# Kernel tuning notes

Hardware: AMD Instinct MI355X
Metric: run time of the kernel (lower is better)

## Reference

```python
import jax, jax.numpy as jnp
import numpy as np
import math

EMBED_DIM = 1024
NUM_HEADS = 16
HEAD_DIM = EMBED_DIM // NUM_HEADS
BATCH = 2
SEQ = 2048


def setup_inputs() -> dict:
    key = jax.random.key(0)
    ks = jax.random.split(key, 9)
    s = 1.0 / math.sqrt(EMBED_DIM)
    return {
        "x": jax.random.normal(ks[0], (BATCH, SEQ, EMBED_DIM), jnp.float32),
        "Wq": jax.random.normal(ks[1], (EMBED_DIM, EMBED_DIM), jnp.float32) * s,
        "bq": jnp.zeros((EMBED_DIM,), jnp.float32),
        "Wk": jax.random.normal(ks[2], (EMBED_DIM, EMBED_DIM), jnp.float32) * s,
        "bk": jnp.zeros((EMBED_DIM,), jnp.float32),
        "Wv": jax.random.normal(ks[3], (EMBED_DIM, EMBED_DIM), jnp.float32) * s,
        "bv": jnp.zeros((EMBED_DIM,), jnp.float32),
        "Wo": jax.random.normal(ks[4], (EMBED_DIM, EMBED_DIM), jnp.float32) * s,
        "bo": jnp.zeros((EMBED_DIM,), jnp.float32),
    }


def _rope_tables(seq_len, dim, dtype):
    inv_freq = 1.0 / (10000.0 ** (jnp.arange(0, dim, 2, dtype=jnp.float32) / dim))
    t = jnp.arange(seq_len, dtype=jnp.float32)
    freqs = jnp.einsum("i,j->ij", t, inv_freq)          # [S, D/2]
    emb = jnp.concatenate([freqs, freqs], axis=-1)       # [S, D]
    return jnp.cos(emb).astype(dtype), jnp.sin(emb).astype(dtype)


def _rotate_half(x):
    x1, x2 = jnp.split(x, 2, axis=-1)
    return jnp.concatenate([-x2, x1], axis=-1)


def _apply_rope(x, cos, sin):
    # x: [B, S, H, D]; cos/sin: [S, D] -> broadcast over batch & heads
    cos = cos[None, :, None, :]
    sin = sin[None, :, None, :]
    return x * cos + _rotate_half(x) * sin


def reference(x, Wq, bq, Wk, bk, Wv, bv, Wo, bo):
    B, S, E = x.shape
    H, D = NUM_HEADS, HEAD_DIM
    q = (x @ Wq + bq).reshape(B, S, H, D)
    k = (x @ Wk + bk).reshape(B, S, H, D)
    v = (x @ Wv + bv).reshape(B, S, H, D)
    cos, sin = _rope_tables(S, D, x.dtype)
    q = _apply_rope(q, cos, sin)
    k = _apply_rope(k, cos, sin)
    scale = 1.0 / math.sqrt(D)
    # scores: [B, H, S, S]
    scores = jnp.einsum("bqhd,bkhd->bhqk", q, k) * scale
    attn = jax.nn.softmax(scores, axis=-1)
    ctx = jnp.einsum("bhqk,bkhd->bqhd", attn, v).reshape(B, S, E)
    return ctx @ Wo + bo
```

## Files before the change

kernel.cpp:

```cpp
#include <hip/hip_runtime.h>
#include <math.h>

#define B_ 2
#define S_ 2048
#define E_ 1024
#define H_ 16
#define D_ 64
#define M_ (B_*S_)

typedef _Float16 f16x8  __attribute__((ext_vector_type(8)));
typedef _Float16 f16x4v __attribute__((ext_vector_type(4)));
typedef __fp16   h16x2  __attribute__((ext_vector_type(2)));
typedef float    f32x4  __attribute__((ext_vector_type(4)));

__device__ __forceinline__ ushort f2h(float f) {
    _Float16 h = (_Float16)f;
    return __builtin_bit_cast(ushort, h);
}

__device__ __forceinline__ void gload_lds16(const ushort* g, ushort* l) {
    __builtin_amdgcn_global_load_lds(
        (const __attribute__((address_space(1))) unsigned int*)g,
        (__attribute__((address_space(3))) unsigned int*)l, 16, 0, 0);
}

__device__ __forceinline__ float exp2_fast(float x) {
    return __builtin_amdgcn_exp2f(x);
}

__global__ void prep_kernel(const float* __restrict__ x,
                            const float* __restrict__ W0, const float* __restrict__ W1,
                            const float* __restrict__ W2, const float* __restrict__ W3,
                            ushort* __restrict__ xf, ushort* __restrict__ WT,
                            float* __restrict__ ct, float* __restrict__ st)
{
    const int bid = blockIdx.x;
    const int tid = threadIdx.x;
    __shared__ float tile[32][33];

    if (bid < 2048) {
        const int z = bid >> 9, rem = bid & 511;
        const int kp = rem >> 5, nb = (rem & 31) * 32;
        const float* W = (z == 0) ? W0 : (z == 1) ? W1 : (z == 2) ? W2 : W3;
        const size_t zoff = (size_t)z * E_ * E_;
        const int tx = tid & 31, ty = tid >> 5;
        #pragma unroll
        for (int kk = 0; kk < 2; kk++) {
            const int k0 = kp * 64 + kk * 32;
            #pragma unroll
            for (int i = 0; i < 4; i++) {
                int r = i * 8 + ty;
                tile[r][tx] = W[(size_t)(k0 + r) * E_ + nb + tx];
            }
            __syncthreads();
            #pragma unroll
            for (int i = 0; i < 4; i++) {
                int r = i * 8 + ty;
                WT[zoff + (size_t)(nb + r) * E_ + k0 + tx] = f2h(tile[tx][r]);
            }
            __syncthreads();
        }
    } else if (bid < 3072) {
        const int base = (bid - 2048) * 4096 + tid * 4;
        #pragma unroll
        for (int j = 0; j < 4; j++) {
            const int i = base + j * 1024;
            float4 v = *(const float4*)&x[i];
            *(ushort4*)&xf[i] = make_ushort4(f2h(v.x), f2h(v.y), f2h(v.z), f2h(v.w));
        }
    } else {
        const int i = (bid - 3072) * 256 + tid;
        const int j = i & 31, pos = i >> 5;
        float invf = (float)pow(10000.0, -(double)j / 32.0);
        float ang  = (float)pos * invf;
        ct[i] = (float)cos((double)ang);
        st[i] = (float)sin((double)ang);
    }
}

#define GBM 128
#define GBN 128
#define GBK 32
#define LOG2E 1.44269504088896340736f

__global__ __launch_bounds__(256, 3)
void gemm_f16(const ushort* __restrict__ A, const ushort* __restrict__ WTp,
              const float* __restrict__ b0, const float* __restrict__ b1,
              const float* __restrict__ b2,
              const float* __restrict__ ct, const float* __restrict__ st,
              ushort* __restrict__ outQ, ushort* __restrict__ outK,
              ushort* __restrict__ outV)
{
    __shared__ __align__(16) ushort lA[3][GBM * GBK];
    __shared__ __align__(16) ushort lB[3][GBN * GBK];

    const int tid  = threadIdx.x;
    const int wv   = tid >> 6, lane = tid & 63;
    const int c    = lane & 15, qd = lane >> 4;
    const int rh   = wv >> 1, chn = wv & 1;

    const int mode = (int)blockIdx.z;
    const size_t zoff = (size_t)blockIdx.z * (E_ * E_);
    const ushort* Bt = WTp + zoff;

    const int m0 = (blockIdx.x & 31) * GBM;
    const int n0 = (blockIdx.x >> 5) * GBN;

    const ushort* gsrc = (wv < 2) ? A : Bt;
    const int rowbase = ((wv < 2) ? m0 : n0) + (wv & 1) * 64;
    const int lofs = (wv & 1) * 64 * GBK;
    const int srow = lane >> 2;
    const int soct = (lane & 3) * 8;

    f32x4 acc[4][4] = {};

    #pragma unroll
    for (int pt = 0; pt < 2; pt++) {
        ushort* dst = ((wv < 2) ? &lA[pt][0] : &lB[pt][0]) + lofs;
        const int k0i = pt * GBK;
        #pragma unroll
        for (int cc = 0; cc < 4; cc++) {
            const ushort* g = gsrc + (size_t)(rowbase + cc * 16 + srow) * E_ + k0i + soct;
            gload_lds16(g, dst + cc * 512);
        }
    }
    __builtin_amdgcn_s_waitcnt(0x0F74);
    __builtin_amdgcn_s_barrier();

    for (int t = 0; t < E_ / GBK; t++) {
        if (t + 2 < E_ / GBK) {
            const int bi = (t + 2) % 3;
            const int k0i = (t + 2) * GBK;
            ushort* dst = ((wv < 2) ? &lA[bi][0] : &lB[bi][0]) + lofs;
            #pragma unroll
            for (int cc = 0; cc < 4; cc++) {
                const ushort* g = gsrc + (size_t)(rowbase + cc * 16 + srow) * E_ + k0i + soct;
                gload_lds16(g, dst + cc * 512);
            }
        }

        const ushort* Ab = lA[t % 3];
        const ushort* Bb = lB[t % 3];

        f16x8 af[4], bf[4];
        #pragma unroll
        for (int mt = 0; mt < 4; mt++)
            af[mt] = *(const f16x8*)&Ab[(rh * 64 + mt * 16 + c) * GBK + qd * 8];
        #pragma unroll
        for (int nt = 0; nt < 4; nt++)
            bf[nt] = *(const f16x8*)&Bb[(chn * 64 + nt * 16 + c) * GBK + qd * 8];
        #pragma unroll
        for (int mt = 0; mt < 4; mt++)
            #pragma unroll
            for (int nt = 0; nt < 4; nt++)
                acc[mt][nt] = __builtin_amdgcn_mfma_f32_16x16x32_f16(af[mt], bf[nt], acc[mt][nt], 0, 0, 0);

        if (t < E_ / GBK - 2) {
            __builtin_amdgcn_s_waitcnt(0x0F74);
            __builtin_amdgcn_s_barrier();
        } else if (t == E_ / GBK - 2) {
            __builtin_amdgcn_s_waitcnt(0x0F70);
            __builtin_amdgcn_s_barrier();
        }
    }

    const float* bias = (mode == 0) ? b0 : (mode == 1) ? b1 : b2;
    const int colbase = n0 + chn * 64;

    if (mode == 2) {
        const int hd = colbase >> 6;
        const int xr = (c >> 2) & 3;
        #pragma unroll
        for (int mt = 0; mt < 4; mt++)
            #pragma unroll
            for (int r = 0; r < 4; r++) {
                const int row = m0 + rh * 64 + mt * 16 + qd * 4 + r;
                const int bb = row >> 11, sl = row & (S_ - 1);
                const int g  = sl >> 5, k32 = sl & 31;
                const int q2 = (k32 >> 2) & 3, kh = k32 >> 4, kj = k32 & 3;
                const size_t base = (size_t)(bb * H_ + hd) * (S_ * D_)
                                  + g * 2048 + ((q2 ^ xr) << 3) + kh * 4 + kj;
                #pragma unroll
                for (int nt = 0; nt < 4; nt++) {
                    const int d = nt * 16 + c;
                    outV[base + (size_t)d * 32] = f2h(acc[mt][nt][r] + bias[colbase + d]);
                }
            }
    } else {
        ushort* O = (mode == 0) ? outQ : outK;
        const float sc = (mode == 0) ? 0.125f * LOG2E : 1.0f;
        #pragma unroll
        for (int mt = 0; mt < 4; mt++)
            #pragma unroll
            for (int r = 0; r < 4; r++) {
                const int row = m0 + rh * 64 + mt * 16 + qd * 4 + r;
                const int pos = row & (S_ - 1);
                const int sw = row & 7;
                #pragma unroll
                for (int p = 0; p < 2; p++) {
                    const int j32 = p * 16 + c;
                    const float cth = ct[pos * 32 + j32], sth = st[pos * 32 + j32];
                    const float v1 = acc[mt][p][r]     + bias[colbase + p * 16 + c];
                    const float v2 = acc[mt][p + 2][r] + bias[colbase + (p + 2) * 16 + c];
                    const float o1 = (v1 * cth - v2 * sth) * sc;
                    const float o2 = (v2 * cth + v1 * sth) * sc;
                    const int cd1 = p * 16 + c, cd2 = cd1 + 32;
                    O[(size_t)row * E_ + colbase + (((cd1 >> 3) ^ sw) * 8) + (cd1 & 7)] = f2h(o1);
                    O[(size_t)row * E_ + colbase + (((cd2 >> 3) ^ sw) * 8) + (cd2 & 7)] = f2h(o2);
                }
            }
    }
}

__global__ __launch_bounds__(256, 3)
void gemm_proj(const ushort* __restrict__ A, const ushort* __restrict__ WTp,
               const float* __restrict__ bo, float* __restrict__ outF)
{
    __shared__ __align__(16) ushort lA[3][64 * GBK];
    __shared__ __align__(16) ushort lB[3][GBN * GBK];

    const int tid  = threadIdx.x;
    const int wv   = tid >> 6, lane = tid & 63;
    const int c    = lane & 15, qd = lane >> 4;

    const int m0 = (blockIdx.x & 63) * 64;
    const int n0 = (blockIdx.x >> 6) * GBN;

    const bool stager = (wv < 3);
    const ushort* gsrc = (wv == 0) ? A : WTp;
    const int rowbase = (wv == 0) ? m0 : (n0 + (wv - 1) * 64);
    const int lofs = (wv == 0) ? 0 : (wv - 1) * 64 * GBK;
    const int srow = lane >> 2;
    const int soct = (lane & 3) * 8;

    f32x4 acc[4][2] = {};

    #pragma unroll
    for (int pt = 0; pt < 2; pt++) {
        if (stager) {
            ushort* dst = ((wv == 0) ? &lA[pt][0] : &lB[pt][0]) + lofs;
            const int k0i = pt * GBK;
            #pragma unroll
            for (int cc = 0; cc < 4; cc++) {
                const ushort* g = gsrc + (size_t)(rowbase + cc * 16 + srow) * E_ + k0i + soct;
                gload_lds16(g, dst + cc * 512);
            }
        }
    }
    __builtin_amdgcn_s_waitcnt(0x0F74);
    __builtin_amdgcn_s_barrier();

    for (int t = 0; t < E_ / GBK; t++) {
        if (t + 2 < E_ / GBK && stager) {
            const int bi = (t + 2) % 3;
            const int k0i = (t + 2) * GBK;
            ushort* dst = ((wv == 0) ? &lA[bi][0] : &lB[bi][0]) + lofs;
            #pragma unroll
            for (int cc = 0; cc < 4; cc++) {
                const ushort* g = gsrc + (size_t)(rowbase + cc * 16 + srow) * E_ + k0i + soct;
                gload_lds16(g, dst + cc * 512);
            }
        }

        const ushort* Ab = lA[t % 3];
        const ushort* Bb = lB[t % 3];

        f16x8 af[4], bf[2];
        #pragma unroll
        for (int mt = 0; mt < 4; mt++)
            af[mt] = *(const f16x8*)&Ab[(mt * 16 + c) * GBK + qd * 8];
        #pragma unroll
        for (int nt = 0; nt < 2; nt++)
            bf[nt] = *(const f16x8*)&Bb[(wv * 32 + nt * 16 + c) * GBK + qd * 8];
        #pragma unroll
        for (int mt = 0; mt < 4; mt++)
            #pragma unroll
            for (int nt = 0; nt < 2; nt++)
                acc[mt][nt] = __builtin_amdgcn_mfma_f32_16x16x32_f16(af[mt], bf[nt], acc[mt][nt], 0, 0, 0);

        if (t < E_ / GBK - 2) {
            __builtin_amdgcn_s_waitcnt(0x0F74);
            __builtin_amdgcn_s_barrier();
        } else if (t == E_ / GBK - 2) {
            __builtin_amdgcn_s_waitcnt(0x0F70);
            __builtin_amdgcn_s_barrier();
        }
    }

    #pragma unroll
    for (int mt = 0; mt < 4; mt++)
        #pragma unroll
        for (int r = 0; r < 4; r++) {
            const int row = m0 + mt * 16 + qd * 4 + r;
            #pragma unroll
            for (int nt = 0; nt < 2; nt++) {
                const int col = n0 + wv * 32 + nt * 16 + c;
                outF[(size_t)row * E_ + col] = acc[mt][nt][r] + bo[col];
            }
        }
}

__global__ __launch_bounds__(256, 3)
void attn_mfma(const ushort* __restrict__ Qf, const ushort* __restrict__ Kf,
               const ushort* __restrict__ Vfg, ushort* __restrict__ ctxf)
{
    __shared__ __align__(16) ushort L[24576];

    const int tid = threadIdx.x;
    const int wv = tid >> 6, lane = tid & 63;
    const int c = lane & 15, qd = lane >> 4;
    const int cs = c & 7;

    const int xcd = blockIdx.x & 7, ii = blockIdx.x >> 3;
    const int bh = xcd * 4 + (ii & 3);
    const int qtb = ii >> 2;
    const int b = bh >> 4, h = bh & 15;
    const int q0 = qtb * 64;

    const size_t qrow0 = (size_t)b * S_ + q0;
    const size_t krow0 = (size_t)b * S_;
    const size_t vbase = (size_t)bh * (S_ * D_);

    const int l8 = lane >> 3, l7 = lane & 7;

    #pragma unroll
    for (int j = 0; j < 2; j++) {
        const int row = wv * 16 + j * 8 + l8;
        gload_lds16(Qf + (qrow0 + row) * E_ + h * 64 + l7 * 8, &L[wv * 1024 + j * 512]);
    }
    __syncthreads();
    f16x8 qfrag[4][2];
    #pragma unroll
    for (int qt = 0; qt < 4; qt++)
        #pragma unroll
        for (int kc = 0; kc < 2; kc++)
            qfrag[qt][kc] = *(const f16x8*)&L[(qt * 16 + c) * 64 + (((kc * 4 + qd) ^ cs) * 8)];
    __syncthreads();

    f32x4 acc[4][4] = {};
    float lsum[4] = {0.f, 0.f, 0.f, 0.f};

    ushort* const myL = &L[wv * 6144];
    const int vxo = (qd ^ ((c >> 2) & 3)) << 3;

    const ushort* kst0 = Kf + (krow0 + wv * 32 + l8) * E_ + h * 64 + l7 * 8;
    const ushort* kst1 = kst0 + 8 * E_;
    const ushort* vstA = Vfg + vbase + (size_t)wv * 2048 + lane * 8;
    const ushort* vstB = vstA + 512;

    gload_lds16(kst0, myL);
    gload_lds16(kst1, myL + 512);
    gload_lds16(vstA, myL + 2048);
    gload_lds16(vstB, myL + 2560);
    kst0 += 16 * E_; kst1 += 16 * E_; vstA += 1024; vstB += 1024;

    #pragma unroll 1
    for (int T = 0; T < 16; T++) {
        uint4 bfu[4];

        {
            ushort* vd = myL + 2048 + (T & 1) * 2048 + 1024;
            gload_lds16(kst0, myL + 1024);
            gload_lds16(kst1, myL + 1536);
            gload_lds16(vstA, vd);
            gload_lds16(vstB, vd + 512);
            kst0 += 112 * E_; kst1 += 112 * E_; vstA += 7168; vstB += 7168;
            __builtin_amdgcn_s_waitcnt(0x0F74);

            const ushort* kb = myL;
            f16x8 kf0 = *(const f16x8*)&kb[c * 64 + ((qd ^ cs) * 8)];
            f16x8 kf1 = *(const f16x8*)&kb[c * 64 + (((4 + qd) ^ cs) * 8)];
            f32x4 sv[4];
            __builtin_amdgcn_s_setprio(1);
            #pragma unroll
            for (int qt = 0; qt < 4; qt++) {
                f32x4 s = {};
                s = __builtin_amdgcn_mfma_f32_16x16x32_f16(kf0, qfrag[qt][0], s, 0, 0, 0);
                sv[qt] = __builtin_amdgcn_mfma_f32_16x16x32_f16(kf1, qfrag[qt][1], s, 0, 0, 0);
            }
            __builtin_amdgcn_s_setprio(0);
            #pragma unroll
            for (int qt = 0; qt < 4; qt++) {
                const float p0 = exp2_fast(sv[qt][0]), p1 = exp2_fast(sv[qt][1]);
                const float p2 = exp2_fast(sv[qt][2]), p3 = exp2_fast(sv[qt][3]);
                lsum[qt] += (p0 + p1) + (p2 + p3);
                bfu[qt].x = __builtin_bit_cast(unsigned int, __builtin_amdgcn_cvt_pkrtz(p0, p1));
                bfu[qt].y = __builtin_bit_cast(unsigned int, __builtin_amdgcn_cvt_pkrtz(p2, p3));
            }
        }

        {
            if (T < 15) {
                ushort* vd = myL + 2048 + ((T + 1) & 1) * 2048;
                gload_lds16(kst0, myL);
                gload_lds16(kst1, myL + 512);
                gload_lds16(vstA, vd);
                gload_lds16(vstB, vd + 512);
                kst0 += 16 * E_; kst1 += 16 * E_; vstA += 1024; vstB += 1024;
                __builtin_amdgcn_s_waitcnt(0x0F74);
            } else {
                __builtin_amdgcn_s_waitcnt(0x0F70);
            }

            const ushort* kb = myL + 1024;
            f16x8 kf0 = *(const f16x8*)&kb[c * 64 + ((qd ^ cs) * 8)];
            f16x8 kf1 = *(const f16x8*)&kb[c * 64 + (((4 + qd) ^ cs) * 8)];
            f32x4 sv[4];
            __builtin_amdgcn_s_setprio(1);
            #pragma unroll
            for (int qt = 0; qt < 4; qt++) {
                f32x4 s = {};
                s = __builtin_amdgcn_mfma_f32_16x16x32_f16(kf0, qfrag[qt][0], s, 0, 0, 0);
                sv[qt] = __builtin_amdgcn_mfma_f32_16x16x32_f16(kf1, qfrag[qt][1], s, 0, 0, 0);
            }
            __builtin_amdgcn_s_setprio(0);
            #pragma unroll
            for (int qt = 0; qt < 4; qt++) {
                const float p0 = exp2_fast(sv[qt][0]), p1 = exp2_fast(sv[qt][1]);
                const float p2 = exp2_fast(sv[qt][2]), p3 = exp2_fast(sv[qt][3]);
                lsum[qt] += (p0 + p1) + (p2 + p3);
                bfu[qt].z = __builtin_bit_cast(unsigned int, __builtin_amdgcn_cvt_pkrtz(p0, p1));
                bfu[qt].w = __builtin_bit_cast(unsigned int, __builtin_amdgcn_cvt_pkrtz(p2, p3));
            }
        }

        const ushort* vb = myL + 2048 + (T & 1) * 2048;
        __builtin_amdgcn_s_setprio(1);
        #pragma unroll
        for (int dt = 0; dt < 4; dt++) {
            f16x8 vfr = *(const f16x8*)&vb[(dt * 16 + c) * 32 + vxo];
            #pragma unroll
            for (int qt = 0; qt < 4; qt++)
                acc[dt][qt] = __builtin_amdgcn_mfma_f32_16x16x32_f16(
                    vfr, __builtin_bit_cast(f16x8, bfu[qt]), acc[dt][qt], 0, 0, 0);
        }
        __builtin_amdgcn_s_setprio(0);
    }

    __syncthreads();

    float* red = (float*)&L[0];
    float* lsr = (float*)&L[8192];

    #pragma unroll
    for (int qt = 0; qt < 4; qt++) {
        float v = lsum[qt];
        v += __shfl_xor(v, 16);
        v += __shfl_xor(v, 32);
        lsum[qt] = v;
    }
    if (lane < 16) {
        #pragma unroll
        for (int qt = 0; qt < 4; qt++) lsr[wv * 64 + qt * 16 + lane] = lsum[qt];
    }

    f32x4 own[4];
    #pragma unroll
    for (int qt = 0; qt < 4; qt++)
        own[qt] = (wv == 0) ? acc[0][qt] : (wv == 1) ? acc[1][qt]
                : (wv == 2) ? acc[2][qt] : acc[3][qt];

    #pragma unroll
    for (int r = 1; r < 4; r++) {
        const int ds = (wv + r) & 3;
        #pragma unroll
        for (int qt = 0; qt < 4; qt++) {
            f32x4 sv = (ds == 0) ? acc[0][qt] : (ds == 1) ? acc[1][qt]
                     : (ds == 2) ? acc[2][qt] : acc[3][qt];
            *(f32x4*)&red[ds * 1024 + qt * 256 + lane * 4] = sv;
        }
        __syncthreads();
        #pragma unroll
        for (int qt = 0; qt < 4; qt++)
            own[qt] += *(const f32x4*)&red[wv * 1024 + qt * 256 + lane * 4];
        if (r < 3) __syncthreads();
    }

    float inv[4];
    #pragma unroll
    for (int qt = 0; qt < 4; qt++) {
        const int q = qt * 16 + c;
        inv[qt] = 1.0f / (lsr[q] + lsr[64 + q] + lsr[128 + q] + lsr[192 + q]);
    }

    const size_t obase = qrow0 * E_ + h * 64 + wv * 16 + qd * 4;
    #pragma unroll
    for (int qt = 0; qt < 4; qt++) {
        f32x4 v = own[qt];
        const float iq = inv[qt];
        ushort4 o = make_ushort4(f2h(v[0] * iq), f2h(v[1] * iq),
                                 f2h(v[2] * iq), f2h(v[3] * iq));
        *(ushort4*)&ctxf[obase + (size_t)(qt * 16 + c) * E_] = o;
    }
}

extern "C" void kernel_launch(void* const* d_in, const int* in_sizes, int n_in,
                              void* d_out, int out_size, void* d_ws, size_t ws_size,
                              hipStream_t stream)
{
    const float* x  = (const float*)d_in[0];
    const float* Wq = (const float*)d_in[1];
    const float* bq = (const float*)d_in[2];
    const float* Wk = (const float*)d_in[3];
    const float* bk = (const float*)d_in[4];
    const float* Wv = (const float*)d_in[5];
    const float* bv = (const float*)d_in[6];
    const float* Wo = (const float*)d_in[7];
    const float* bo = (const float*)d_in[8];
    float* out = (float*)d_out;

    ushort* Qb = (ushort*)d_ws;
    ushort* Kb = Qb + (size_t)M_ * E_;
    ushort* Vf = Kb + (size_t)M_ * E_;
    ushort* xf = Vf + (size_t)M_ * E_;
    ushort* WT = xf + (size_t)M_ * E_;
    float*  ct = (float*)(WT + (size_t)4 * E_ * E_);
    float*  st = ct + S_ * 32;
    ushort* ctxf = Qb;

    hipLaunchKernelGGL(prep_kernel, dim3(3328), dim3(256), 0, stream,
                       x, Wq, Wk, Wv, Wo, xf, WT, ct, st);

    hipLaunchKernelGGL(gemm_f16, dim3(256, 1, 3), dim3(256), 0, stream,
                       xf, WT, bq, bk, bv, ct, st,
                       Qb, Kb, Vf);

    hipLaunchKernelGGL(attn_mfma, dim3(B_ * H_ * (S_ / 64)), dim3(256), 0, stream,
                       Qb, Kb, Vf, ctxf);

    hipLaunchKernelGGL(gemm_proj, dim3(512), dim3(256), 0, stream,
                       ctxf, WT + (size_t)3 * E_ * E_, bo, out);
}
```

Measured before the change: 180.8 us.

## Halve attention query tile to 32 rows and single-buffer V for higher occupancy

The attention kernel now processes 32 query rows per block instead of 64, which doubles the grid. The V tile moves from double to single buffering, cutting LDS per block from 48KB to 32KB and raising launch bounds to 4 blocks per CU. The next V tile is now loaded only after the PV MFMAs finish, which exposes V load latency within each iteration. Each K/V tile is also reused across fewer queries, so K and V global/L2 traffic doubles. The intent is better latency hiding through occupancy, traded against less reuse.

```diff
diff --git a/kernel.cpp b/kernel.cpp
--- a/kernel.cpp
+++ b/kernel.cpp
@@ -300,11 +300,11 @@
         }
 }
 
-__global__ __launch_bounds__(256, 3)
+__global__ __launch_bounds__(256, 4)
 void attn_mfma(const ushort* __restrict__ Qf, const ushort* __restrict__ Kf,
                const ushort* __restrict__ Vfg, ushort* __restrict__ ctxf)
 {
-    __shared__ __align__(16) ushort L[24576];
+    __shared__ __align__(16) ushort L[16384];
 
     const int tid = threadIdx.x;
     const int wv = tid >> 6, lane = tid & 63;
@@ -315,7 +315,7 @@
     const int bh = xcd * 4 + (ii & 3);
     const int qtb = ii >> 2;
     const int b = bh >> 4, h = bh & 15;
-    const int q0 = qtb * 64;
+    const int q0 = qtb * 32;
 
     const size_t qrow0 = (size_t)b * S_ + q0;
     const size_t krow0 = (size_t)b * S_;
@@ -323,24 +323,20 @@
 
     const int l8 = lane >> 3, l7 = lane & 7;
 
-    #pragma unroll
-    for (int j = 0; j < 2; j++) {
-        const int row = wv * 16 + j * 8 + l8;
-        gload_lds16(Qf + (qrow0 + row) * E_ + h * 64 + l7 * 8, &L[wv * 1024 + j * 512]);
-    }
+    gload_lds16(Qf + (qrow0 + wv * 8 + l8) * E_ + h * 64 + l7 * 8, &L[wv * 512]);
     __syncthreads();
-    f16x8 qfrag[4][2];
-    #pragma unroll
-    for (int qt = 0; qt < 4; qt++)
+    f16x8 qfrag[2][2];
+    #pragma unroll
+    for (int qt = 0; qt < 2; qt++)
         #pragma unroll
         for (int kc = 0; kc < 2; kc++)
             qfrag[qt][kc] = *(const f16x8*)&L[(qt * 16 + c) * 64 + (((kc * 4 + qd) ^ cs) * 8)];
     __syncthreads();
 
-    f32x4 acc[4][4] = {};
-    float lsum[4] = {0.f, 0.f, 0.f, 0.f};
-
-    ushort* const myL = &L[wv * 6144];
+    f32x4 acc[4][2] = {};
+    float lsum[2] = {0.f, 0.f};
+
+    ushort* const myL = &L[wv * 4096];
     const int vxo = (qd ^ ((c >> 2) & 3)) << 3;
 
     const ushort* kst0 = Kf + (krow0 + wv * 32 + l8) * E_ + h * 64 + l7 * 8;
@@ -350,37 +346,38 @@
 
     gload_lds16(kst0, myL);
     gload_lds16(kst1, myL + 512);
+    kst0 += 16 * E_; kst1 += 16 * E_;
     gload_lds16(vstA, myL + 2048);
     gload_lds16(vstB, myL + 2560);
-    kst0 += 16 * E_; kst1 += 16 * E_; vstA += 1024; vstB += 1024;
+    vstA += 1024; vstB += 1024;
+    gload_lds16(vstA, myL + 3072);
+    gload_lds16(vstB, myL + 3584);
+    vstA += 7168; vstB += 7168;
 
     #pragma unroll 1
     for (int T = 0; T < 16; T++) {
-        uint4 bfu[4];
+        uint4 bfu[2];
 
         {
-            ushort* vd = myL + 2048 + (T & 1) * 2048 + 1024;
             gload_lds16(kst0, myL + 1024);
             gload_lds16(kst1, myL + 1536);
-            gload_lds16(vstA, vd);
-            gload_lds16(vstB, vd + 512);
-            kst0 += 112 * E_; kst1 += 112 * E_; vstA += 7168; vstB += 7168;
-            __builtin_amdgcn_s_waitcnt(0x0F74);
+            kst0 += 112 * E_; kst1 += 112 * E_;
+            __builtin_amdgcn_s_waitcnt(0x0F76);
 
             const ushort* kb = myL;
             f16x8 kf0 = *(const f16x8*)&kb[c * 64 + ((qd ^ cs) * 8)];
             f16x8 kf1 = *(const f16x8*)&kb[c * 64 + (((4 + qd) ^ cs) * 8)];
-            f32x4 sv[4];
+            f32x4 sv[2];
             __builtin_amdgcn_s_setprio(1);
             #pragma unroll
-            for (int qt = 0; qt < 4; qt++) {
+            for (int qt = 0; qt < 2; qt++) {
                 f32x4 s = {};
                 s = __builtin_amdgcn_mfma_f32_16x16x32_f16(kf0, qfrag[qt][0], s, 0, 0, 0);
                 sv[qt] = __builtin_amdgcn_mfma_f32_16x16x32_f16(kf1, qfrag[qt][1], s, 0, 0, 0);
             }
             __builtin_amdgcn_s_setprio(0);
             #pragma unroll
-            for (int qt = 0; qt < 4; qt++) {
+            for (int qt = 0; qt < 2; qt++) {
                 const float p0 = exp2_fast(sv[qt][0]), p1 = exp2_fast(sv[qt][1]);
                 const float p2 = exp2_fast(sv[qt][2]), p3 = exp2_fast(sv[qt][3]);
                 lsum[qt] += (p0 + p1) + (p2 + p3);
@@ -391,13 +388,10 @@
 
         {
             if (T < 15) {
-                ushort* vd = myL + 2048 + ((T + 1) & 1) * 2048;
                 gload_lds16(kst0, myL);
                 gload_lds16(kst1, myL + 512);
-                gload_lds16(vstA, vd);
-                gload_lds16(vstB, vd + 512);
-                kst0 += 16 * E_; kst1 += 16 * E_; vstA += 1024; vstB += 1024;
-                __builtin_amdgcn_s_waitcnt(0x0F74);
+                kst0 += 16 * E_; kst1 += 16 * E_;
+                __builtin_amdgcn_s_waitcnt(0x0F72);
             } else {
                 __builtin_amdgcn_s_waitcnt(0x0F70);
             }
@@ -405,17 +399,17 @@
             const ushort* kb = myL + 1024;
             f16x8 kf0 = *(const f16x8*)&kb[c * 64 + ((qd ^ cs) * 8)];
             f16x8 kf1 = *(const f16x8*)&kb[c * 64 + (((4 + qd) ^ cs) * 8)];
-            f32x4 sv[4];
+            f32x4 sv[2];
             __builtin_amdgcn_s_setprio(1);
             #pragma unroll
-            for (int qt = 0; qt < 4; qt++) {
+            for (int qt = 0; qt < 2; qt++) {
                 f32x4 s = {};
                 s = __builtin_amdgcn_mfma_f32_16x16x32_f16(kf0, qfrag[qt][0], s, 0, 0, 0);
                 sv[qt] = __builtin_amdgcn_mfma_f32_16x16x32_f16(kf1, qfrag[qt][1], s, 0, 0, 0);
             }
             __builtin_amdgcn_s_setprio(0);
             #pragma unroll
-            for (int qt = 0; qt < 4; qt++) {
+            for (int qt = 0; qt < 2; qt++) {
                 const float p0 = exp2_fast(sv[qt][0]), p1 = exp2_fast(sv[qt][1]);
                 const float p2 = exp2_fast(sv[qt][2]), p3 = exp2_fast(sv[qt][3]);
                 lsum[qt] += (p0 + p1) + (p2 + p3);
@@ -424,26 +418,36 @@
             }
         }
 
-        const ushort* vb = myL + 2048 + (T & 1) * 2048;
+        const ushort* vb = myL + 2048;
         __builtin_amdgcn_s_setprio(1);
         #pragma unroll
         for (int dt = 0; dt < 4; dt++) {
             f16x8 vfr = *(const f16x8*)&vb[(dt * 16 + c) * 32 + vxo];
-            #pragma unroll
-            for (int qt = 0; qt < 4; qt++)
-                acc[dt][qt] = __builtin_amdgcn_mfma_f32_16x16x32_f16(
-                    vfr, __builtin_bit_cast(f16x8, bfu[qt]), acc[dt][qt], 0, 0, 0);
+            acc[dt][0] = __builtin_amdgcn_mfma_f32_16x16x32_f16(
+                vfr, __builtin_bit_cast(f16x8, bfu[0]), acc[dt][0], 0, 0, 0);
+            acc[dt][1] = __builtin_amdgcn_mfma_f32_16x16x32_f16(
+                vfr, __builtin_bit_cast(f16x8, bfu[1]), acc[dt][1], 0, 0, 0);
         }
         __builtin_amdgcn_s_setprio(0);
+
+        if (T < 15) {
+            __builtin_amdgcn_sched_barrier(0);
+            gload_lds16(vstA, myL + 2048);
+            gload_lds16(vstB, myL + 2560);
+            vstA += 1024; vstB += 1024;
+            gload_lds16(vstA, myL + 3072);
+            gload_lds16(vstB, myL + 3584);
+            vstA += 7168; vstB += 7168;
+        }
     }
 
     __syncthreads();
 
     float* red = (float*)&L[0];
-    float* lsr = (float*)&L[8192];
-
-    #pragma unroll
-    for (int qt = 0; qt < 4; qt++) {
+    float* lsr = (float*)&L[4096];
+
+    #pragma unroll
+    for (int qt = 0; qt < 2; qt++) {
         float v = lsum[qt];
         v += __shfl_xor(v, 16);
         v += __shfl_xor(v, 32);
@@ -451,12 +455,12 @@
     }
     if (lane < 16) {
         #pragma unroll
-        for (int qt = 0; qt < 4; qt++) lsr[wv * 64 + qt * 16 + lane] = lsum[qt];
-    }
-
-    f32x4 own[4];
-    #pragma unroll
-    for (int qt = 0; qt < 4; qt++)
+        for (int qt = 0; qt < 2; qt++) lsr[wv * 32 + qt * 16 + lane] = lsum[qt];
+    }
+
+    f32x4 own[2];
+    #pragma unroll
+    for (int qt = 0; qt < 2; qt++)
         own[qt] = (wv == 0) ? acc[0][qt] : (wv == 1) ? acc[1][qt]
                 : (wv == 2) ? acc[2][qt] : acc[3][qt];
 
@@ -464,28 +468,28 @@
     for (int r = 1; r < 4; r++) {
         const int ds = (wv + r) & 3;
         #pragma unroll
-        for (int qt = 0; qt < 4; qt++) {
+        for (int qt = 0; qt < 2; qt++) {
             f32x4 sv = (ds == 0) ? acc[0][qt] : (ds == 1) ? acc[1][qt]
                      : (ds == 2) ? acc[2][qt] : acc[3][qt];
-            *(f32x4*)&red[ds * 1024 + qt * 256 + lane * 4] = sv;
+            *(f32x4*)&red[ds * 512 + qt * 256 + lane * 4] = sv;
         }
         __syncthreads();
         #pragma unroll
-        for (int qt = 0; qt < 4; qt++)
-            own[qt] += *(const f32x4*)&red[wv * 1024 + qt * 256 + lane * 4];
+        for (int qt = 0; qt < 2; qt++)
+            own[qt] += *(const f32x4*)&red[wv * 512 + qt * 256 + lane * 4];
         if (r < 3) __syncthreads();
     }
 
-    float inv[4];
-    #pragma unroll
-    for (int qt = 0; qt < 4; qt++) {
+    float inv[2];
+    #pragma unroll
+    for (int qt = 0; qt < 2; qt++) {
         const int q = qt * 16 + c;
-        inv[qt] = 1.0f / (lsr[q] + lsr[64 + q] + lsr[128 + q] + lsr[192 + q]);
+        inv[qt] = 1.0f / (lsr[q] + lsr[32 + q] + lsr[64 + q] + lsr[96 + q]);
     }
 
     const size_t obase = qrow0 * E_ + h * 64 + wv * 16 + qd * 4;
     #pragma unroll
-    for (int qt = 0; qt < 4; qt++) {
+    for (int qt = 0; qt < 2; qt++) {
         f32x4 v = own[qt];
         const float iq = inv[qt];
         ushort4 o = make_ushort4(f2h(v[0] * iq), f2h(v[1] * iq),
@@ -525,7 +529,7 @@
                        xf, WT, bq, bk, bv, ct, st,
                        Qb, Kb, Vf);
 
-    hipLaunchKernelGGL(attn_mfma, dim3(B_ * H_ * (S_ / 64)), dim3(256), 0, stream,
+    hipLaunchKernelGGL(attn_mfma, dim3(B_ * H_ * (S_ / 32)), dim3(256), 0, stream,
                        Qb, Kb, Vf, ctxf);
 
     hipLaunchKernelGGL(gemm_proj, dim3(512), dim3(256), 0, stream,
```

Measured after the change: 200.7 us. +11.0%, slower.

## Single-buffer K/V in LDS, reissuing loads right after fragment reads

Applied to the files above, without the earlier changes.

Shrinks the attention kernel's LDS from 48KB to 32KB by removing V double-buffering. Each K half-tile and the V tile now use one slot, and the next prefetch is issued as soon as the fragments are in registers (waitcnt on LDS reads plus a sched_barrier). The intent is higher occupancy, or less LDS pressure at three blocks per CU, while keeping loads overlapped with the MFMA work. The trade-off is a shorter prefetch distance, so waits on global loads may be exposed and the hand-tuned waitcnt encodings must match the new load order.

```diff
diff --git a/kernel.cpp b/kernel.cpp
--- a/kernel.cpp
+++ b/kernel.cpp
@@ -304,7 +304,7 @@
 void attn_mfma(const ushort* __restrict__ Qf, const ushort* __restrict__ Kf,
                const ushort* __restrict__ Vfg, ushort* __restrict__ ctxf)
 {
-    __shared__ __align__(16) ushort L[24576];
+    __shared__ __align__(16) ushort L[16384];
 
     const int tid = threadIdx.x;
     const int wv = tid >> 6, lane = tid & 63;
@@ -340,7 +340,7 @@
     f32x4 acc[4][4] = {};
     float lsum[4] = {0.f, 0.f, 0.f, 0.f};
 
-    ushort* const myL = &L[wv * 6144];
+    ushort* const myL = &L[wv * 4096];
     const int vxo = (qd ^ ((c >> 2) & 3)) << 3;
 
     const ushort* kst0 = Kf + (krow0 + wv * 32 + l8) * E_ + h * 64 + l7 * 8;
@@ -350,26 +350,33 @@
 
     gload_lds16(kst0, myL);
     gload_lds16(kst1, myL + 512);
+    kst0 += 16 * E_; kst1 += 16 * E_;
+    gload_lds16(kst0, myL + 1024);
+    gload_lds16(kst1, myL + 1536);
+    kst0 += 112 * E_; kst1 += 112 * E_;
     gload_lds16(vstA, myL + 2048);
     gload_lds16(vstB, myL + 2560);
-    kst0 += 16 * E_; kst1 += 16 * E_; vstA += 1024; vstB += 1024;
+    vstA += 1024; vstB += 1024;
+    gload_lds16(vstA, myL + 3072);
+    gload_lds16(vstB, myL + 3584);
+    vstA += 7168; vstB += 7168;
 
     #pragma unroll 1
     for (int T = 0; T < 16; T++) {
         uint4 bfu[4];
 
         {
-            ushort* vd = myL + 2048 + (T & 1) * 2048 + 1024;
-            gload_lds16(kst0, myL + 1024);
-            gload_lds16(kst1, myL + 1536);
-            gload_lds16(vstA, vd);
-            gload_lds16(vstB, vd + 512);
-            kst0 += 112 * E_; kst1 += 112 * E_; vstA += 7168; vstB += 7168;
-            __builtin_amdgcn_s_waitcnt(0x0F74);
-
+            __builtin_amdgcn_s_waitcnt(0x0F76);
             const ushort* kb = myL;
             f16x8 kf0 = *(const f16x8*)&kb[c * 64 + ((qd ^ cs) * 8)];
             f16x8 kf1 = *(const f16x8*)&kb[c * 64 + (((4 + qd) ^ cs) * 8)];
+            __builtin_amdgcn_s_waitcnt(0xC07F);
+            __builtin_amdgcn_sched_barrier(0);
+            if (T < 15) {
+                gload_lds16(kst0, myL);
+                gload_lds16(kst1, myL + 512);
+                kst0 += 16 * E_; kst1 += 16 * E_;
+            }
             f32x4 sv[4];
             __builtin_amdgcn_s_setprio(1);
             #pragma unroll
@@ -390,21 +397,18 @@
         }
 
         {
-            if (T < 15) {
-                ushort* vd = myL + 2048 + ((T + 1) & 1) * 2048;
-                gload_lds16(kst0, myL);
-                gload_lds16(kst1, myL + 512);
-                gload_lds16(vstA, vd);
-                gload_lds16(vstB, vd + 512);
-                kst0 += 16 * E_; kst1 += 16 * E_; vstA += 1024; vstB += 1024;
-                __builtin_amdgcn_s_waitcnt(0x0F74);
-            } else {
-                __builtin_amdgcn_s_waitcnt(0x0F70);
-            }
-
+            if (T < 15) __builtin_amdgcn_s_waitcnt(0x0F76);
+            else        __builtin_amdgcn_s_waitcnt(0x0F74);
             const ushort* kb = myL + 1024;
             f16x8 kf0 = *(const f16x8*)&kb[c * 64 + ((qd ^ cs) * 8)];
             f16x8 kf1 = *(const f16x8*)&kb[c * 64 + (((4 + qd) ^ cs) * 8)];
+            __builtin_amdgcn_s_waitcnt(0xC07F);
+            __builtin_amdgcn_sched_barrier(0);
+            if (T < 15) {
+                gload_lds16(kst0, myL + 1024);
+                gload_lds16(kst1, myL + 1536);
+                kst0 += 112 * E_; kst1 += 112 * E_;
+            }
             f32x4 sv[4];
             __builtin_amdgcn_s_setprio(1);
             #pragma unroll
@@ -424,17 +428,35 @@
             }
         }
 
-        const ushort* vb = myL + 2048 + (T & 1) * 2048;
-        __builtin_amdgcn_s_setprio(1);
-        #pragma unroll
-        for (int dt = 0; dt < 4; dt++) {
-            f16x8 vfr = *(const f16x8*)&vb[(dt * 16 + c) * 32 + vxo];
-            #pragma unroll
-            for (int qt = 0; qt < 4; qt++)
-                acc[dt][qt] = __builtin_amdgcn_mfma_f32_16x16x32_f16(
-                    vfr, __builtin_bit_cast(f16x8, bfu[qt]), acc[dt][qt], 0, 0, 0);
-        }
-        __builtin_amdgcn_s_setprio(0);
+        {
+            if (T < 15) __builtin_amdgcn_s_waitcnt(0x0F74);
+            else        __builtin_amdgcn_s_waitcnt(0x0F70);
+            const ushort* vb = myL + 2048;
+            f16x8 vf0 = *(const f16x8*)&vb[(0 * 16 + c) * 32 + vxo];
+            f16x8 vf1 = *(const f16x8*)&vb[(1 * 16 + c) * 32 + vxo];
+            f16x8 vf2 = *(const f16x8*)&vb[(2 * 16 + c) * 32 + vxo];
+            f16x8 vf3 = *(const f16x8*)&vb[(3 * 16 + c) * 32 + vxo];
+            __builtin_amdgcn_s_waitcnt(0xC07F);
+            __builtin_amdgcn_sched_barrier(0);
+            if (T < 15) {
+                gload_lds16(vstA, myL + 2048);
+                gload_lds16(vstB, myL + 2560);
+                vstA += 1024; vstB += 1024;
+                gload_lds16(vstA, myL + 3072);
+                gload_lds16(vstB, myL + 3584);
+                vstA += 7168; vstB += 7168;
+            }
+            __builtin_amdgcn_s_setprio(1);
+            #pragma unroll
+            for (int qt = 0; qt < 4; qt++) {
+                const f16x8 pb = __builtin_bit_cast(f16x8, bfu[qt]);
+                acc[0][qt] = __builtin_amdgcn_mfma_f32_16x16x32_f16(vf0, pb, acc[0][qt], 0, 0, 0);
+                acc[1][qt] = __builtin_amdgcn_mfma_f32_16x16x32_f16(vf1, pb, acc[1][qt], 0, 0, 0);
+                acc[2][qt] = __builtin_amdgcn_mfma_f32_16x16x32_f16(vf2, pb, acc[2][qt], 0, 0, 0);
+                acc[3][qt] = __builtin_amdgcn_mfma_f32_16x16x32_f16(vf3, pb, acc[3][qt], 0, 0, 0);
+            }
+            __builtin_amdgcn_s_setprio(0);
+        }
     }
 
     __syncthreads();
```

After: 183.1 us. Within noise of the previous version (+1.3%).
